# Performance work log

Hardware: AMD Instinct MI355X
Metric: run time of the kernel (lower is better)

Reference implementation:

```python
import jax, jax.numpy as jnp
import numpy as np

STRIDES = (8.0, 16.0, 32.0)
REG_MAX = 7
TOP_K = 100          # top_k_n: max per class and max total
NMS_PRE = 1000       # hardcoded prefilter in get_bboxes
IOU_THRES = 0.5      # literal passed to combined_non_max_suppression
BOX_SCORE = 0.3
IMG_SIZE = (640.0, 640.0)


def _centers(h, w, stride):
    # row-major (h, w) flatten, points stored as (y, x)
    y = (jnp.arange(h, dtype=jnp.float32) + 0.5) * stride
    x = (jnp.arange(w, dtype=jnp.float32) + 0.5) * stride
    return jnp.stack([jnp.repeat(y, w), jnp.tile(x, h)], axis=-1)  # [h*w, 2]


def _distribution(bbox_pred, stride):
    # softmax over reg_max+1 bins -> expected distance, scaled by stride
    b = bbox_pred.shape[0]
    p = jax.nn.softmax(bbox_pred.reshape(b, -1, REG_MAX + 1), axis=-1)
    ln = jnp.arange(REG_MAX + 1, dtype=jnp.float32)
    d = jnp.einsum('bnk,k->bn', p, ln).reshape(b, -1, 4)
    return d * stride


def _process_level(cls_score, bbox_pred, stride):
    b, h, w, c = cls_score.shape
    scores = jax.nn.sigmoid(cls_score.reshape(b, h * w, c))
    dist = _distribution(bbox_pred, stride)                     # [b, hw, 4]
    pts = jnp.broadcast_to(_centers(h, w, stride)[None], (b, h * w, 2))
    if h * w > NMS_PRE:  # static shape check, mirrors TF graph specialization
        max_scores = jnp.max(scores, axis=-1)                   # [b, hw]
        _, topk = jax.lax.top_k(max_scores, NMS_PRE)            # [b, NMS_PRE]
        scores = jnp.take_along_axis(scores, topk[..., None], axis=1)
        dist = jnp.take_along_axis(dist, topk[..., None], axis=1)
        pts = jnp.take_along_axis(pts, topk[..., None], axis=1)
    # distance2bbox with clipping to model input shape
    y1 = jnp.clip(pts[..., 0] - dist[..., 0], 0.0, IMG_SIZE[0])
    x1 = jnp.clip(pts[..., 1] - dist[..., 1], 0.0, IMG_SIZE[1])
    y2 = jnp.clip(pts[..., 0] + dist[..., 2], 0.0, IMG_SIZE[0])
    x2 = jnp.clip(pts[..., 1] + dist[..., 3], 0.0, IMG_SIZE[1])
    return jnp.stack([y1, x1, y2, x2], axis=-1), scores


def _iou_1_vs_n(box, boxes):
    yy1 = jnp.maximum(box[0], boxes[:, 0])
    xx1 = jnp.maximum(box[1], boxes[:, 1])
    yy2 = jnp.minimum(box[2], boxes[:, 2])
    xx2 = jnp.minimum(box[3], boxes[:, 3])
    inter = jnp.maximum(yy2 - yy1, 0.0) * jnp.maximum(xx2 - xx1, 0.0)
    a1 = (box[2] - box[0]) * (box[3] - box[1])
    a2 = (boxes[:, 2] - boxes[:, 0]) * (boxes[:, 3] - boxes[:, 1])
    return inter / (a1 + a2 - inter + 1e-9)


def _nms_single(boxes, scores):
    # greedy NMS, fixed TOP_K iterations; boxes [N,4], scores [N]
    def step(s, _):
        i = jnp.argmax(s)
        sc = s[i]
        suppress = _iou_1_vs_n(boxes[i], boxes) > IOU_THRES
        s = jnp.where(suppress, -jnp.inf, s)
        s = s.at[i].set(-jnp.inf)
        return s, (i, sc)
    _, (idx, sel) = jax.lax.scan(step, scores, None, length=TOP_K)
    return idx, sel  # [TOP_K] each


def _combined_nms(boxes, scores):
    # per-class NMS then global top-K, emulating tf.image.combined_non_max_suppression
    n, c = scores.shape
    idx, sel = jax.vmap(_nms_single, in_axes=(None, 1))(boxes, scores)  # [C, K]
    sel_boxes = boxes[idx]                                              # [C, K, 4]
    cls = jnp.broadcast_to(jnp.arange(c, dtype=jnp.float32)[:, None], (c, TOP_K))
    flat_s = sel.reshape(-1)
    flat_s = jnp.where(jnp.isfinite(flat_s), flat_s, -1.0)
    top_s, top_i = jax.lax.top_k(flat_s, TOP_K)
    out_boxes = sel_boxes.reshape(-1, 4)[top_i]
    out_cls = cls.reshape(-1)[top_i]
    ok = top_s > -1.0
    out_s = jnp.where(ok, top_s, 0.0)
    out_boxes = jnp.where(ok[:, None], out_boxes, 0.0)
    out_cls = jnp.where(ok, out_cls, 0.0)
    return out_boxes, out_s, out_cls


def setup_inputs() -> dict:
    key = jax.random.key(0)
    ks = jax.random.split(key, 7)
    b, c = 16, 20
    inp = {}
    for i, hw in enumerate((80, 40, 20)):
        inp[f'cls_score_{i}'] = jax.random.normal(ks[i], (b, hw, hw, c), dtype=jnp.float32)
        inp[f'bbox_pred_{i}'] = jax.random.normal(ks[3 + i], (b, hw, hw, 4 * (REG_MAX + 1)), dtype=jnp.float32)
    inp['origin_shapes'] = jax.random.uniform(ks[6], (b, 2), dtype=jnp.float32) * 1280.0
    return inp


def reference(cls_score_0, cls_score_1, cls_score_2,
              bbox_pred_0, bbox_pred_1, bbox_pred_2, origin_shapes):
    cls_scores = (cls_score_0, cls_score_1, cls_score_2)
    bbox_preds = (bbox_pred_0, bbox_pred_1, bbox_pred_2)
    mlvl_b, mlvl_s = [], []
    for cs, bp, st in zip(cls_scores, bbox_preds, STRIDES):
        bb, sc = _process_level(cs, bp, st)
        mlvl_b.append(bb)
        mlvl_s.append(sc)
    boxes = jnp.concatenate(mlvl_b, axis=1)    # [B, 2400, 4]
    scores = jnp.concatenate(mlvl_s, axis=1)   # [B, 2400, C]
    nb, ns, nc = jax.vmap(_combined_nms)(boxes, scores)
    out = jnp.concatenate([nb, ns[..., None], nc[..., None]], axis=-1)  # [B, K, 6]
    mask = (ns > BOX_SCORE).astype(out.dtype)
    return out * mask[..., None]
```

## Files before the change

### kernel.cpp

```cpp
#include <hip/hip_runtime.h>
#include <math.h>

#define BATCH 16
#define NCLS 20
#define TOPK 100
#define NPRE 1000
#define NTOT 2400
#define NBINS 8
#define N0 6400
#define N1 1600
#define SSEL 256

#define MID05 0.50000002980232238769531250

__device__ __forceinline__ unsigned int orderable(float x) {
    unsigned int u = __float_as_uint(x);
    return (u & 0x80000000u) ? ~u : (u | 0x80000000u);
}
__device__ __forceinline__ float unorderable(unsigned int k) {
    return __uint_as_float((k & 0x80000000u) ? (k ^ 0x80000000u) : ~k);
}

__global__ __launch_bounds__(256) void compute_keys_kernel(
        const float* __restrict__ cls0, const float* __restrict__ cls1,
        unsigned int* __restrict__ keys0, unsigned int* __restrict__ keys1) {
    int tg = blockIdx.x * 256 + threadIdx.x;
    const float* p;
    unsigned int* dst;
    if (tg < BATCH * N0) {
        p = cls0 + (size_t)tg * NCLS;
        dst = keys0 + tg;
    } else {
        int a = tg - BATCH * N0;
        if (a >= BATCH * N1) return;
        p = cls1 + (size_t)a * NCLS;
        dst = keys1 + a;
    }
    const float4* p4 = (const float4*)p;
    float m = -INFINITY;
    #pragma unroll
    for (int q = 0; q < 5; ++q) {
        float4 v = p4[q];
        m = fmaxf(m, fmaxf(fmaxf(v.x, v.y), fmaxf(v.z, v.w)));
    }
    *dst = orderable(m);
}

__global__ __launch_bounds__(256) void radix_select_kernel(
        const unsigned int* __restrict__ keys0, const unsigned int* __restrict__ keys1,
        int* __restrict__ sel_idx) {
    int bid = blockIdx.x;
    int b = bid >> 1;
    int lvl = bid & 1;
    int n = (lvl == 0) ? N0 : N1;
    const unsigned int* gk = (lvl == 0 ? keys0 : keys1) + (size_t)b * n;

    __shared__ unsigned int skey[N0];
    __shared__ unsigned int hist[256];
    __shared__ unsigned int sfxA[257], sfxB[257];
    __shared__ int eq[256];
    __shared__ unsigned int s_prefix, s_kk, s_cnt, s_eqcnt;
    int t = threadIdx.x;

    for (int a = t; a < n; a += 256) skey[a] = gk[a];
    if (t == 0) {
        s_kk = NPRE; s_prefix = 0u; s_cnt = 0u; s_eqcnt = 0u;
        sfxA[256] = 0u; sfxB[256] = 0u;
    }
    __syncthreads();

    for (int pass = 0; pass < 4; ++pass) {
        int shift = 24 - 8 * pass;
        hist[t] = 0u;
        __syncthreads();
        unsigned int prefix = s_prefix, kk = s_kk;
        for (int a = t; a < n; a += 256) {
            unsigned int u = skey[a];
            if (pass == 0 || (u >> (shift + 8)) == prefix)
                atomicAdd(&hist[(u >> shift) & 255u], 1u);
        }
        __syncthreads();
        sfxA[t] = hist[t];
        __syncthreads();
        unsigned int* src = sfxA; unsigned int* dst = sfxB;
        #pragma unroll
        for (int step = 1; step < 256; step <<= 1) {
            int idx = t + step; if (idx > 256) idx = 256;
            dst[t] = src[t] + src[idx];
            __syncthreads();
            unsigned int* tmp = src; src = dst; dst = tmp;
        }
        unsigned int Sd = src[t];
        unsigned int Sd1 = src[t + 1];
        if (Sd >= kk && Sd1 < kk) {
            s_prefix = (prefix << 8) | (unsigned int)t;
            s_kk = kk - Sd1;
        }
        __syncthreads();
    }

    unsigned int T = s_prefix;
    int* out = sel_idx + b * 2000 + lvl * 1000;
    for (int a = t; a < n; a += 256) {
        unsigned int u = skey[a];
        if (u > T) {
            unsigned int pos = atomicAdd(&s_cnt, 1u);
            out[pos] = a;
        } else if (u == T) {
            unsigned int p = atomicAdd(&s_eqcnt, 1u);
            if (p < 256u) eq[p] = a;
        }
    }
    __syncthreads();
    if (t == 0) {
        unsigned int pos = s_cnt;
        unsigned int rem = s_kk;
        unsigned int cnt = s_eqcnt;
        if (cnt <= 256u) {
            for (unsigned int i = 1; i < cnt; ++i) {
                int key = eq[i]; int j2 = (int)i - 1;
                while (j2 >= 0 && eq[j2] > key) { eq[j2 + 1] = eq[j2]; --j2; }
                eq[j2 + 1] = key;
            }
            for (unsigned int i = 0; i < rem; ++i) out[pos + i] = eq[i];
        } else {
            for (int a = 0; a < n && rem > 0u; ++a)
                if (skey[a] == T) { out[pos++] = a; --rem; }
        }
    }
}

__global__ __launch_bounds__(256) void decode_kernel(
        const float* __restrict__ cls0, const float* __restrict__ cls1, const float* __restrict__ cls2,
        const float* __restrict__ bb0,  const float* __restrict__ bb1,  const float* __restrict__ bb2,
        const int* __restrict__ sel_idx,
        float* __restrict__ boxes_all, float* __restrict__ scores_t) {
    int tg = blockIdx.x * blockDim.x + threadIdx.x;
    if (tg >= BATCH * NTOT) return;
    int b = tg / NTOT, j = tg % NTOT;

    const float* cls; const float* bb; int a, w; float stride;
    if (j < 1000) {
        a = sel_idx[b * 2000 + j]; w = 80; stride = 8.f;
        cls = cls0 + ((size_t)b * N0 + a) * NCLS;
        bb  = bb0  + ((size_t)b * N0 + a) * 32;
    } else if (j < 2000) {
        a = sel_idx[b * 2000 + j]; w = 40; stride = 16.f;
        cls = cls1 + ((size_t)b * N1 + a) * NCLS;
        bb  = bb1  + ((size_t)b * N1 + a) * 32;
    } else {
        a = j - 2000; w = 20; stride = 32.f;
        cls = cls2 + ((size_t)b * 400 + a) * NCLS;
        bb  = bb2  + ((size_t)b * 400 + a) * 32;
    }

    float cl[20];
    {
        const float4* c4 = (const float4*)cls;
        #pragma unroll
        for (int q = 0; q < 5; ++q) *(float4*)&cl[q * 4] = c4[q];
    }
    float bl[32];
    {
        const float4* b4 = (const float4*)bb;
        #pragma unroll
        for (int q = 0; q < 8; ++q) *(float4*)&bl[q * 4] = b4[q];
    }

    #pragma unroll
    for (int c = 0; c < NCLS; ++c)
        scores_t[((size_t)b * NCLS + c) * NTOT + j] = 1.f / (1.f + expf(-cl[c]));

    float d[4];
    #pragma unroll
    for (int s = 0; s < 4; ++s) {
        const float* l = &bl[s * NBINS];
        float m = l[0];
        #pragma unroll
        for (int k = 1; k < NBINS; ++k) m = fmaxf(m, l[k]);
        float e[NBINS], sum = 0.f;
        #pragma unroll
        for (int k = 0; k < NBINS; ++k) { e[k] = expf(l[k] - m); sum += e[k]; }
        float acc = 0.f;
        #pragma unroll
        for (int k = 0; k < NBINS; ++k) acc += (e[k] / sum) * (float)k;
        d[s] = acc * stride;
    }
    float cy = ((float)(a / w) + 0.5f) * stride;
    float cx = ((float)(a % w) + 0.5f) * stride;
    float* bx = boxes_all + ((size_t)b * NTOT + j) * 4;
    bx[0] = fminf(fmaxf(cy - d[0], 0.f), 640.f);
    bx[1] = fminf(fmaxf(cx - d[1], 0.f), 640.f);
    bx[2] = fminf(fmaxf(cy + d[2], 0.f), 640.f);
    bx[3] = fminf(fmaxf(cx + d[3], 0.f), 640.f);
}

__global__ __launch_bounds__(256) void class_nms_kernel(
        const float* __restrict__ boxes_all, const float* __restrict__ scores_t,
        float* __restrict__ nms_score, int* __restrict__ nms_idx) {
    int blk = blockIdx.x;
    int b = blk / NCLS;
    int t = threadIdx.x;

    __shared__ unsigned int skey[NTOT];
    __shared__ unsigned int hist[256];
    __shared__ unsigned int sfxA[257], sfxB[257];
    __shared__ int eq[128];
    __shared__ unsigned int s_prefix, s_kk, s_cnt, s_eqcnt;
    __shared__ unsigned long long sorted[SSEL];
    __shared__ float4 abox[TOPK];
    __shared__ float4 cbox[64];
    __shared__ int s_outPos;
    __shared__ unsigned long long s_m;

    const float*  ssrc = scores_t + (size_t)blk * NTOT;
    const float4* bsrc = (const float4*)boxes_all + (size_t)b * NTOT;
    float* osc = nms_score + (size_t)blk * TOPK;
    int*   oid = nms_idx   + (size_t)blk * TOPK;

    for (int j = t; j < NTOT; j += 256) skey[j] = orderable(ssrc[j]);
    if (t == 0) {
        s_kk = SSEL; s_prefix = 0u; s_cnt = 0u; s_eqcnt = 0u;
        sfxA[256] = 0u; sfxB[256] = 0u; s_outPos = 0;
    }
    __syncthreads();

    for (int pass = 0; pass < 4; ++pass) {
        int shift = 24 - 8 * pass;
        hist[t] = 0u;
        __syncthreads();
        unsigned int prefix = s_prefix, kk = s_kk;
        for (int j = t; j < NTOT; j += 256) {
            unsigned int u = skey[j];
            if (pass == 0 || (u >> (shift + 8)) == prefix)
                atomicAdd(&hist[(u >> shift) & 255u], 1u);
        }
        __syncthreads();
        sfxA[t] = hist[t];
        __syncthreads();
        unsigned int* src = sfxA; unsigned int* dst = sfxB;
        #pragma unroll
        for (int step = 1; step < 256; step <<= 1) {
            int idx = t + step; if (idx > 256) idx = 256;
            dst[t] = src[t] + src[idx];
            __syncthreads();
            unsigned int* tmp = src; src = dst; dst = tmp;
        }
        unsigned int Sd = src[t];
        unsigned int Sd1 = src[t + 1];
        if (Sd >= kk && Sd1 < kk) {
            s_prefix = (prefix << 8) | (unsigned int)t;
            s_kk = kk - Sd1;
        }
        __syncthreads();
    }

    unsigned int T = s_prefix;
    for (int j = t; j < NTOT; j += 256) {
        unsigned int u = skey[j];
        if (u > T) {
            unsigned int pos = atomicAdd(&s_cnt, 1u);
            sorted[pos] = ((unsigned long long)u << 32) | (unsigned int)~j;
        } else if (u == T) {
            unsigned int p = atomicAdd(&s_eqcnt, 1u);
            if (p < 128u) eq[p] = j;
        }
    }
    __syncthreads();
    if (t == 0) {
        unsigned int pos = s_cnt;
        unsigned int rem = s_kk;
        unsigned int cnt = s_eqcnt;
        if (cnt <= 128u) {
            for (unsigned int i = 1; i < cnt; ++i) {
                int key = eq[i]; int j2 = (int)i - 1;
                while (j2 >= 0 && eq[j2] > key) { eq[j2 + 1] = eq[j2]; --j2; }
                eq[j2 + 1] = key;
            }
            for (unsigned int i = 0; i < rem; ++i)
                sorted[pos + i] = ((unsigned long long)T << 32) | (unsigned int)~eq[i];
        } else {
            for (int j = 0; j < NTOT && rem > 0u; ++j)
                if (skey[j] == T) {
                    sorted[pos++] = ((unsigned long long)T << 32) | (unsigned int)~j;
                    --rem;
                }
        }
    }
    __syncthreads();

    for (int k2 = 2; k2 <= SSEL; k2 <<= 1) {
        for (int j2 = k2 >> 1; j2 > 0; j2 >>= 1) {
            int l = t ^ j2;
            if (l > t && t < SSEL) {
                bool asc = ((t & k2) == 0);
                unsigned long long a = sorted[t], bb2 = sorted[l];
                if ((a > bb2) == asc) { sorted[t] = bb2; sorted[l] = a; }
            }
            __syncthreads();
        }
    }

    if (t < 64) {
        int lane = t;
        int outPos = 0;
        for (int chunk = 0; chunk < SSEL / 64 && outPos < TOPK; ++chunk) {
            unsigned long long key = sorted[SSEL - 1 - (chunk * 64 + lane)];
            unsigned int j = ~(unsigned int)key;
            float sc = unorderable((unsigned int)(key >> 32));
            float4 bj = bsrc[j];
            cbox[lane] = bj;
            float amine = (bj.z - bj.x) * (bj.w - bj.y);

            bool sup = false;
            for (int t2 = 0; t2 < outPos; ++t2) {
                float4 wb = abox[t2];
                float a1 = (wb.z - wb.x) * (wb.w - wb.y);
                float yy1 = fmaxf(wb.x, bj.x);
                float xx1 = fmaxf(wb.y, bj.y);
                float yy2 = fminf(wb.z, bj.z);
                float xx2 = fminf(wb.w, bj.w);
                float inter = fmaxf(yy2 - yy1, 0.f) * fmaxf(xx2 - xx1, 0.f);
                float denom = a1 + amine - inter + 1e-9f;
                sup = sup || ((double)inter > MID05 * (double)denom);
            }

            unsigned long long supmask = 0ull;
            #pragma unroll 8
            for (int j2 = 0; j2 < 64; ++j2) {
                float4 wb = cbox[j2];
                float a1 = (wb.z - wb.x) * (wb.w - wb.y);
                float yy1 = fmaxf(wb.x, bj.x);
                float xx1 = fmaxf(wb.y, bj.y);
                float yy2 = fminf(wb.z, bj.z);
                float xx2 = fminf(wb.w, bj.w);
                float inter = fmaxf(yy2 - yy1, 0.f) * fmaxf(xx2 - xx1, 0.f);
                float denom = a1 + amine - inter + 1e-9f;
                bool s2 = ((double)inter > MID05 * (double)denom);
                if (s2 && j2 < lane) supmask |= (1ull << j2);
            }

            unsigned long long cand = __ballot(!sup);
            unsigned long long accbits = 0ull;
            while (cand) {
                int i = __builtin_ctzll(cand);
                accbits |= (1ull << i);
                cand &= ~(1ull << i);
                unsigned long long row = __ballot((supmask >> i) & 1ull);
                cand &= ~row;
            }

            int nAcc = (int)__builtin_popcountll(accbits);
            int avail = TOPK - outPos;
            bool mine = (accbits >> lane) & 1ull;
            int myrank = (int)__builtin_popcountll(accbits & ((1ull << lane) - 1ull));
            if (mine && myrank < avail) {
                int pos = outPos + myrank;
                osc[pos] = sc;
                oid[pos] = (int)j;
                abox[pos] = bj;
            }
            outPos += (nAcc < avail) ? nAcc : avail;
            __builtin_amdgcn_s_waitcnt(0);
        }
        if (lane == 0) s_outPos = outPos;
    }
    __syncthreads();

    int outPos = s_outPos;
    if (outPos < TOPK) {
        if (t < SSEL) skey[~(unsigned int)sorted[t]] = 0u;
        __syncthreads();
        for (int j = t; j < NTOT; j += 256) {
            unsigned int u = skey[j];
            if (!u) continue;
            float4 bj = bsrc[j];
            float amine = (bj.z - bj.x) * (bj.w - bj.y);
            bool sup = false;
            for (int t2 = 0; t2 < outPos; ++t2) {
                float4 wb = abox[t2];
                float a1 = (wb.z - wb.x) * (wb.w - wb.y);
                float yy1 = fmaxf(wb.x, bj.x);
                float xx1 = fmaxf(wb.y, bj.y);
                float yy2 = fminf(wb.z, bj.z);
                float xx2 = fminf(wb.w, bj.w);
                float inter = fmaxf(yy2 - yy1, 0.f) * fmaxf(xx2 - xx1, 0.f);
                float denom = a1 + amine - inter + 1e-9f;
                sup = sup || ((double)inter > MID05 * (double)denom);
            }
            if (sup) skey[j] = 0u;
        }
        __syncthreads();
        while (outPos < TOPK) {
            if (t == 0) s_m = 0ull;
            __syncthreads();
            unsigned long long loc = 0ull;
            for (int j = t; j < NTOT; j += 256) {
                unsigned int u = skey[j];
                if (u) {
                    unsigned long long kk = ((unsigned long long)u << 32) | (unsigned int)~j;
                    loc = (kk > loc) ? kk : loc;
                }
            }
            atomicMax(&s_m, loc);
            __syncthreads();
            unsigned long long m = s_m;
            if ((long long)m >= 0) break;
            unsigned int wi = ~(unsigned int)m;
            float4 wb = bsrc[wi];
            if (t == 0) {
                osc[outPos] = unorderable((unsigned int)(m >> 32));
                oid[outPos] = (int)wi;
                skey[wi] = 0u;
            }
            __syncthreads();
            float a1 = (wb.z - wb.x) * (wb.w - wb.y);
            for (int j = t; j < NTOT; j += 256) {
                unsigned int u = skey[j];
                if (!u) continue;
                float4 bj = bsrc[j];
                float yy1 = fmaxf(wb.x, bj.x);
                float xx1 = fmaxf(wb.y, bj.y);
                float yy2 = fminf(wb.z, bj.z);
                float xx2 = fminf(wb.w, bj.w);
                float inter = fmaxf(yy2 - yy1, 0.f) * fmaxf(xx2 - xx1, 0.f);
                float a2 = (bj.z - bj.x) * (bj.w - bj.y);
                float denom = a1 + a2 - inter + 1e-9f;
                if ((double)inter > MID05 * (double)denom) skey[j] = 0u;
            }
            ++outPos;
            __syncthreads();
        }
    }

    for (int k2 = outPos + t; k2 < TOPK; k2 += 256) { osc[k2] = -INFINITY; oid[k2] = 0; }
}

__global__ __launch_bounds__(256) void final_topk_kernel(
        const float* __restrict__ nms_score, const int* __restrict__ nms_idx,
        const float* __restrict__ boxes_all, float* __restrict__ out) {
    int b = blockIdx.x, t = threadIdx.x;
    __shared__ unsigned int fkey[2000];
    __shared__ unsigned int hist[256];
    __shared__ unsigned int sfxA[257], sfxB[257];
    __shared__ int eq[128];
    __shared__ unsigned long long fk[128];
    __shared__ unsigned int s_prefix, s_kk, s_cnt, s_eqcnt;

    for (int f = t; f < 2000; f += 256) {
        float s = nms_score[(size_t)b * 2000 + f];
        float v = isfinite(s) ? s : -1.0f;
        fkey[f] = orderable(v);
    }
    if (t == 0) {
        s_kk = TOPK; s_prefix = 0u; s_cnt = 0u; s_eqcnt = 0u;
        sfxA[256] = 0u; sfxB[256] = 0u;
    }
    if (t < 128) fk[t] = 0ull;
    __syncthreads();

    for (int pass = 0; pass < 4; ++pass) {
        int shift = 24 - 8 * pass;
        hist[t] = 0u;
        __syncthreads();
        unsigned int prefix = s_prefix, kk = s_kk;
        for (int f = t; f < 2000; f += 256) {
            unsigned int u = fkey[f];
            if (pass == 0 || (u >> (shift + 8)) == prefix)
                atomicAdd(&hist[(u >> shift) & 255u], 1u);
        }
        __syncthreads();
        sfxA[t] = hist[t];
        __syncthreads();
        unsigned int* src = sfxA; unsigned int* dst = sfxB;
        #pragma unroll
        for (int step = 1; step < 256; step <<= 1) {
            int idx = t + step; if (idx > 256) idx = 256;
            dst[t] = src[t] + src[idx];
            __syncthreads();
            unsigned int* tmp = src; src = dst; dst = tmp;
        }
        unsigned int Sd = src[t];
        unsigned int Sd1 = src[t + 1];
        if (Sd >= kk && Sd1 < kk) {
            s_prefix = (prefix << 8) | (unsigned int)t;
            s_kk = kk - Sd1;
        }
        __syncthreads();
    }

    unsigned int T = s_prefix;
    for (int f = t; f < 2000; f += 256) {
        unsigned int u = fkey[f];
        if (u > T) {
            unsigned int pos = atomicAdd(&s_cnt, 1u);
            fk[pos] = ((unsigned long long)u << 32) | (unsigned int)~f;
        } else if (u == T) {
            unsigned int p = atomicAdd(&s_eqcnt, 1u);
            if (p < 128u) eq[p] = f;
        }
    }
    __syncthreads();
    if (t == 0) {
        unsigned int pos = s_cnt;
        unsigned int rem = s_kk;
        unsigned int cnt = s_eqcnt;
        if (cnt <= 128u) {
            for (unsigned int i = 1; i < cnt; ++i) {
                int key = eq[i]; int j2 = (int)i - 1;
                while (j2 >= 0 && eq[j2] > key) { eq[j2 + 1] = eq[j2]; --j2; }
                eq[j2 + 1] = key;
            }
            for (unsigned int i = 0; i < rem; ++i)
                fk[pos + i] = ((unsigned long long)T << 32) | (unsigned int)~eq[i];
        } else {
            for (int f = 0; f < 2000 && rem > 0u; ++f)
                if (fkey[f] == T) {
                    fk[pos++] = ((unsigned long long)T << 32) | (unsigned int)~f;
                    --rem;
                }
        }
    }
    __syncthreads();

    for (int k2 = 2; k2 <= 128; k2 <<= 1) {
        for (int j2 = k2 >> 1; j2 > 0; j2 >>= 1) {
            if (t < 128) {
                int l = t ^ j2;
                if (l > t) {
                    bool asc = ((t & k2) == 0);
                    unsigned long long a = fk[t], bb2 = fk[l];
                    if ((a > bb2) == asc) { fk[t] = bb2; fk[l] = a; }
                }
            }
            __syncthreads();
        }
    }

    if (t < TOPK) {
        unsigned long long kk = fk[127 - t];
        float v = unorderable((unsigned int)(kk >> 32));
        int fi = (int)~(unsigned int)kk;
        float* o = out + ((size_t)b * TOPK + t) * 6;
        if (v > 0.3f) {
            int bidx = nms_idx[(size_t)b * 2000 + fi];
            float4 bxw = ((const float4*)boxes_all)[(size_t)b * NTOT + bidx];
            o[0] = bxw.x; o[1] = bxw.y; o[2] = bxw.z; o[3] = bxw.w;
            o[4] = v; o[5] = (float)(fi / TOPK);
        } else {
            o[0] = 0.f; o[1] = 0.f; o[2] = 0.f; o[3] = 0.f; o[4] = 0.f; o[5] = 0.f;
        }
    }
}

extern "C" void kernel_launch(void* const* d_in, const int* in_sizes, int n_in,
                              void* d_out, int out_size, void* d_ws, size_t ws_size,
                              hipStream_t stream) {
    (void)out_size; (void)ws_size;
    const float* cls[3] = {nullptr, nullptr, nullptr};
    const float* bbx[3] = {nullptr, nullptr, nullptr};
    for (int i = 0; i < n_in; ++i) {
        const float* p = (const float*)d_in[i];
        switch (in_sizes[i]) {
            case 16 * 6400 * 20: cls[0] = p; break;
            case 16 * 6400 * 32: bbx[0] = p; break;
            case 16 * 1600 * 20: cls[1] = p; break;
            case 16 * 1600 * 32: bbx[1] = p; break;
            case 16 *  400 * 20: cls[2] = p; break;
            case 16 *  400 * 32: bbx[2] = p; break;
            default: break;
        }
    }

    char* w = (char*)d_ws;
    int*   sel_idx    = (int*)(w);
    float* boxes_all  = (float*)(w + 131072);
    float* scores_t   = (float*)(w + 745472);
    unsigned int* keys0 = (unsigned int*)(w + 745472);
    unsigned int* keys1 = (unsigned int*)(w + 745472 + 409600);
    float* nms_score  = (float*)(w + 3817472);
    int*   nms_idx    = (int*)(w + 3945472);

    hipLaunchKernelGGL(compute_keys_kernel, dim3((BATCH * (N0 + N1) + 255) / 256), dim3(256), 0, stream,
                       cls[0], cls[1], keys0, keys1);
    hipLaunchKernelGGL(radix_select_kernel, dim3(32), dim3(256), 0, stream,
                       keys0, keys1, sel_idx);
    hipLaunchKernelGGL(decode_kernel, dim3((BATCH * NTOT + 255) / 256), dim3(256), 0, stream,
                       cls[0], cls[1], cls[2], bbx[0], bbx[1], bbx[2],
                       sel_idx, boxes_all, scores_t);
    hipLaunchKernelGGL(class_nms_kernel, dim3(BATCH * NCLS), dim3(256), 0, stream,
                       boxes_all, scores_t, nms_score, nms_idx);
    hipLaunchKernelGGL(final_topk_kernel, dim3(BATCH), dim3(256), 0, stream,
                       nms_score, nms_idx, boxes_all, (float*)d_out);
}
```

Measured before the change: 156.2 us.

## Replace shared-memory radix scan and bitonic sorts with wavefront shuffle versions

Measured after the change: 153.5 us. About the same (-1.7%).

```diff
diff --git a/kernel.cpp b/kernel.cpp
--- a/kernel.cpp
+++ b/kernel.cpp
@@ -19,6 +19,40 @@
 }
 __device__ __forceinline__ float unorderable(unsigned int k) {
     return __uint_as_float((k & 0x80000000u) ? (k ^ 0x80000000u) : ~k);
+}
+
+__device__ __forceinline__ void radix_pass_scan(
+        const unsigned int* hist, unsigned int* s_prefix, unsigned int* s_kk,
+        unsigned int prefix, unsigned int kk, int t) {
+    if (t < 64) {
+        uint4 h = *(const uint4*)&hist[t * 4];
+        unsigned int s3 = h.w;
+        unsigned int s2 = h.z + s3;
+        unsigned int s1 = h.y + s2;
+        unsigned int s0 = h.x + s1;
+        unsigned int S = s0;
+        #pragma unroll
+        for (int off = 1; off < 64; off <<= 1) {
+            unsigned int o = __shfl_down(S, off);
+            S += (t + off < 64) ? o : 0u;
+        }
+        unsigned int Sgt = S - s0;
+        unsigned int F0 = s0 + Sgt, F1 = s1 + Sgt, F2 = s2 + Sgt, F3 = s3 + Sgt;
+        if (F0 >= kk && F1 < kk)  { *s_prefix = (prefix << 8) | (unsigned int)(t * 4 + 0); *s_kk = kk - F1; }
+        if (F1 >= kk && F2 < kk)  { *s_prefix = (prefix << 8) | (unsigned int)(t * 4 + 1); *s_kk = kk - F2; }
+        if (F2 >= kk && F3 < kk)  { *s_prefix = (prefix << 8) | (unsigned int)(t * 4 + 2); *s_kk = kk - F3; }
+        if (F3 >= kk && Sgt < kk) { *s_prefix = (prefix << 8) | (unsigned int)(t * 4 + 3); *s_kk = kk - Sgt; }
+    }
+}
+
+__device__ __forceinline__ unsigned long long bmerge_shfl(
+        unsigned long long v, int t, int k2, int jmax) {
+    for (int j2 = jmax; j2 > 0; j2 >>= 1) {
+        unsigned long long o = __shfl_xor(v, j2);
+        bool km = (((t & k2) == 0) == ((t & j2) != 0));
+        v = km ? (v > o ? v : o) : (v < o ? v : o);
+    }
+    return v;
 }
 
 __global__ __launch_bounds__(256) void compute_keys_kernel(
@@ -56,46 +90,27 @@
     const unsigned int* gk = (lvl == 0 ? keys0 : keys1) + (size_t)b * n;
 
     __shared__ unsigned int skey[N0];
-    __shared__ unsigned int hist[256];
-    __shared__ unsigned int sfxA[257], sfxB[257];
+    __shared__ __align__(16) unsigned int hist[256];
     __shared__ int eq[256];
     __shared__ unsigned int s_prefix, s_kk, s_cnt, s_eqcnt;
     int t = threadIdx.x;
 
     for (int a = t; a < n; a += 256) skey[a] = gk[a];
-    if (t == 0) {
-        s_kk = NPRE; s_prefix = 0u; s_cnt = 0u; s_eqcnt = 0u;
-        sfxA[256] = 0u; sfxB[256] = 0u;
-    }
+    if (t == 0) { s_kk = NPRE; s_prefix = 0u; s_cnt = 0u; s_eqcnt = 0u; }
     __syncthreads();
 
     for (int pass = 0; pass < 4; ++pass) {
         int shift = 24 - 8 * pass;
+        unsigned int prefix = s_prefix, kk = s_kk;
         hist[t] = 0u;
         __syncthreads();
-        unsigned int prefix = s_prefix, kk = s_kk;
         for (int a = t; a < n; a += 256) {
             unsigned int u = skey[a];
             if (pass == 0 || (u >> (shift + 8)) == prefix)
                 atomicAdd(&hist[(u >> shift) & 255u], 1u);
         }
         __syncthreads();
-        sfxA[t] = hist[t];
-        __syncthreads();
-        unsigned int* src = sfxA; unsigned int* dst = sfxB;
-        #pragma unroll
-        for (int step = 1; step < 256; step <<= 1) {
-            int idx = t + step; if (idx > 256) idx = 256;
-            dst[t] = src[t] + src[idx];
-            __syncthreads();
-            unsigned int* tmp = src; src = dst; dst = tmp;
-        }
-        unsigned int Sd = src[t];
-        unsigned int Sd1 = src[t + 1];
-        if (Sd >= kk && Sd1 < kk) {
-            s_prefix = (prefix << 8) | (unsigned int)t;
-            s_kk = kk - Sd1;
-        }
+        radix_pass_scan(hist, &s_prefix, &s_kk, prefix, kk, t);
         __syncthreads();
     }
 
@@ -203,8 +218,7 @@
     int t = threadIdx.x;
 
     __shared__ unsigned int skey[NTOT];
-    __shared__ unsigned int hist[256];
-    __shared__ unsigned int sfxA[257], sfxB[257];
+    __shared__ __align__(16) unsigned int hist[256];
     __shared__ int eq[128];
     __shared__ unsigned int s_prefix, s_kk, s_cnt, s_eqcnt;
     __shared__ unsigned long long sorted[SSEL];
@@ -219,39 +233,21 @@
     int*   oid = nms_idx   + (size_t)blk * TOPK;
 
     for (int j = t; j < NTOT; j += 256) skey[j] = orderable(ssrc[j]);
-    if (t == 0) {
-        s_kk = SSEL; s_prefix = 0u; s_cnt = 0u; s_eqcnt = 0u;
-        sfxA[256] = 0u; sfxB[256] = 0u; s_outPos = 0;
-    }
+    if (t == 0) { s_kk = SSEL; s_prefix = 0u; s_cnt = 0u; s_eqcnt = 0u; s_outPos = 0; }
     __syncthreads();
 
     for (int pass = 0; pass < 4; ++pass) {
         int shift = 24 - 8 * pass;
+        unsigned int prefix = s_prefix, kk = s_kk;
         hist[t] = 0u;
         __syncthreads();
-        unsigned int prefix = s_prefix, kk = s_kk;
         for (int j = t; j < NTOT; j += 256) {
             unsigned int u = skey[j];
             if (pass == 0 || (u >> (shift + 8)) == prefix)
                 atomicAdd(&hist[(u >> shift) & 255u], 1u);
         }
         __syncthreads();
-        sfxA[t] = hist[t];
-        __syncthreads();
-        unsigned int* src = sfxA; unsigned int* dst = sfxB;
-        #pragma unroll
-        for (int step = 1; step < 256; step <<= 1) {
-            int idx = t + step; if (idx > 256) idx = 256;
-            dst[t] = src[t] + src[idx];
-            __syncthreads();
-            unsigned int* tmp = src; src = dst; dst = tmp;
-        }
-        unsigned int Sd = src[t];
-        unsigned int Sd1 = src[t + 1];
-        if (Sd >= kk && Sd1 < kk) {
-            s_prefix = (prefix << 8) | (unsigned int)t;
-            s_kk = kk - Sd1;
-        }
+        radix_pass_scan(hist, &s_prefix, &s_kk, prefix, kk, t);
         __syncthreads();
     }
 
@@ -289,16 +285,39 @@
     }
     __syncthreads();
 
-    for (int k2 = 2; k2 <= SSEL; k2 <<= 1) {
-        for (int j2 = k2 >> 1; j2 > 0; j2 >>= 1) {
-            int l = t ^ j2;
-            if (l > t && t < SSEL) {
-                bool asc = ((t & k2) == 0);
-                unsigned long long a = sorted[t], bb2 = sorted[l];
-                if ((a > bb2) == asc) { sorted[t] = bb2; sorted[l] = a; }
-            }
-            __syncthreads();
-        }
+    {
+        unsigned long long v = sorted[t];
+        #pragma unroll
+        for (int k2 = 2; k2 <= 64; k2 <<= 1)
+            v = bmerge_shfl(v, t, k2, k2 >> 1);
+        sorted[t] = v;
+        __syncthreads();
+        {
+            unsigned long long o = sorted[t ^ 64];
+            bool km = (((t & 128) == 0) == ((t & 64) != 0));
+            v = km ? (v > o ? v : o) : (v < o ? v : o);
+            v = bmerge_shfl(v, t, 128, 32);
+        }
+        __syncthreads();
+        sorted[t] = v;
+        __syncthreads();
+        {
+            unsigned long long o = sorted[t ^ 128];
+            bool km = ((t & 128) != 0);
+            v = km ? (v > o ? v : o) : (v < o ? v : o);
+        }
+        __syncthreads();
+        sorted[t] = v;
+        __syncthreads();
+        {
+            unsigned long long o = sorted[t ^ 64];
+            bool km = ((t & 64) != 0);
+            v = km ? (v > o ? v : o) : (v < o ? v : o);
+            v = bmerge_shfl(v, t, 256, 32);
+        }
+        __syncthreads();
+        sorted[t] = v;
+        __syncthreads();
     }
 
     if (t < 64) {
@@ -441,8 +460,7 @@
         const float* __restrict__ boxes_all, float* __restrict__ out) {
     int b = blockIdx.x, t = threadIdx.x;
     __shared__ unsigned int fkey[2000];
-    __shared__ unsigned int hist[256];
-    __shared__ unsigned int sfxA[257], sfxB[257];
+    __shared__ __align__(16) unsigned int hist[256];
     __shared__ int eq[128];
     __shared__ unsigned long long fk[128];
     __shared__ unsigned int s_prefix, s_kk, s_cnt, s_eqcnt;
@@ -452,40 +470,22 @@
         float v = isfinite(s) ? s : -1.0f;
         fkey[f] = orderable(v);
     }
-    if (t == 0) {
-        s_kk = TOPK; s_prefix = 0u; s_cnt = 0u; s_eqcnt = 0u;
-        sfxA[256] = 0u; sfxB[256] = 0u;
-    }
+    if (t == 0) { s_kk = TOPK; s_prefix = 0u; s_cnt = 0u; s_eqcnt = 0u; }
     if (t < 128) fk[t] = 0ull;
     __syncthreads();
 
     for (int pass = 0; pass < 4; ++pass) {
         int shift = 24 - 8 * pass;
+        unsigned int prefix = s_prefix, kk = s_kk;
         hist[t] = 0u;
         __syncthreads();
-        unsigned int prefix = s_prefix, kk = s_kk;
         for (int f = t; f < 2000; f += 256) {
             unsigned int u = fkey[f];
             if (pass == 0 || (u >> (shift + 8)) == prefix)
                 atomicAdd(&hist[(u >> shift) & 255u], 1u);
         }
         __syncthreads();
-        sfxA[t] = hist[t];
-        __syncthreads();
-        unsigned int* src = sfxA; unsigned int* dst = sfxB;
-        #pragma unroll
-        for (int step = 1; step < 256; step <<= 1) {
-            int idx = t + step; if (idx > 256) idx = 256;
-            dst[t] = src[t] + src[idx];
-            __syncthreads();
-            unsigned int* tmp = src; src = dst; dst = tmp;
-        }
-        unsigned int Sd = src[t];
-        unsigned int Sd1 = src[t + 1];
-        if (Sd >= kk && Sd1 < kk) {
-            s_prefix = (prefix << 8) | (unsigned int)t;
-            s_kk = kk - Sd1;
-        }
+        radix_pass_scan(hist, &s_prefix, &s_kk, prefix, kk, t);
         __syncthreads();
     }
 
@@ -523,18 +523,24 @@
     }
     __syncthreads();
 
-    for (int k2 = 2; k2 <= 128; k2 <<= 1) {
-        for (int j2 = k2 >> 1; j2 > 0; j2 >>= 1) {
-            if (t < 128) {
-                int l = t ^ j2;
-                if (l > t) {
-                    bool asc = ((t & k2) == 0);
-                    unsigned long long a = fk[t], bb2 = fk[l];
-                    if ((a > bb2) == asc) { fk[t] = bb2; fk[l] = a; }
-                }
-            }
-            __syncthreads();
-        }
+    {
+        unsigned long long v = (t < 128) ? fk[t] : 0ull;
+        if (t < 128) {
+            #pragma unroll
+            for (int k2 = 2; k2 <= 64; k2 <<= 1)
+                v = bmerge_shfl(v, t, k2, k2 >> 1);
+            fk[t] = v;
+        }
+        __syncthreads();
+        if (t < 128) {
+            unsigned long long o = fk[t ^ 64];
+            bool km = ((t & 64) != 0);
+            v = km ? (v > o ? v : o) : (v < o ? v : o);
+            v = bmerge_shfl(v, t, 128, 32);
+        }
+        __syncthreads();
+        if (t < 128) fk[t] = v;
+        __syncthreads();
     }
 
     if (t < TOPK) {
```
